# Performance work log

Hardware: AMD Instinct MI355X
Metric: run time of the kernel (lower is better)

## Reference

```python
import jax, jax.numpy as jnp
import numpy as np
import math

B, L, H, NH, DH = 2, 2048, 1024, 16, 64  # batch, seq, hidden, heads, head dim


def setup_inputs() -> dict:
    key = jax.random.key(0)
    ks = jax.random.split(key, 12)
    s = 0.02
    return {
        "v": jax.random.normal(ks[0], (B, L, H), jnp.float32),
        "k": jax.random.normal(ks[1], (B, L, H), jnp.float32),
        "q": jax.random.normal(ks[2], (B, L, H), jnp.float32),
        "mask": jnp.zeros((B, 1, 1, L), jnp.bool_),
        "Wv": jax.random.normal(ks[3], (H, H), jnp.float32) * s,
        "bv": jnp.zeros((H,), jnp.float32),
        "Wk": jax.random.normal(ks[4], (H, H), jnp.float32) * s,
        "bk": jnp.zeros((H,), jnp.float32),
        "Wq": jax.random.normal(ks[5], (H, H), jnp.float32) * s,
        "bq": jnp.zeros((H,), jnp.float32),
        "Wt": jax.random.normal(ks[6], (H, 1), jnp.float32) * s,
        "bt": jnp.zeros((1,), jnp.float32),
        "Wm": jax.random.normal(ks[7], (H, H), jnp.float32) * s,
        "bm": jnp.zeros((H,), jnp.float32),
    }


def reference(v, k, q, mask, Wv, bv, Wk, bk, Wq, bq, Wt, bt, Wm, bm):
    vp = (v @ Wv + bv).reshape(B, L, NH, DH).transpose(0, 2, 1, 3)  # [B,NH,L,DH]
    kp = k @ Wk + bk  # [B,L,H]
    qp = q @ Wq + bq  # [B,L,H]
    threshold = (qp * kp) @ Wt + bt  # [B,L,1] learned per-position gate threshold
    kh = kp.reshape(B, L, NH, DH).transpose(0, 2, 1, 3)  # [B,NH,L,DH]
    qh = qp.reshape(B, L, NH, DH).transpose(0, 2, 1, 3)
    scores = jnp.einsum("bhqd,bhkd->bhqk", qh, kh) / math.sqrt(DH)
    scores = jnp.where(mask, -1e9, scores)
    att_map = jax.nn.softmax(scores, axis=-1)  # [B,NH,Lq,Lk]
    # column sums: over queries (axis -2) then over heads -> [B,Lk,1]
    colsum = att_map.sum(axis=2).sum(axis=1)[..., None]
    a = (colsum - threshold) > 0  # [B,L,1] boolean gate
    atted = jnp.einsum("bhqk,bhkd->bhqd", att_map, vp)  # [B,NH,L,DH]
    atted = atted.transpose(0, 2, 1, 3).reshape(B, L, H)
    atted = atted * a.astype(atted.dtype)
    return atted @ Wm + bm
```

## Files before the change

### kernel.cpp

```cpp
#include <hip/hip_runtime.h>
#include <math.h>

#define BATCH 2
#define SEQ   2048
#define HID   1024
#define NHEAD 16
#define DHEAD 64
#define MROWS (BATCH*SEQ)
#define SCALE_LOG2E 0.1803368801111244f

typedef __attribute__((ext_vector_type(8))) short short8;
typedef __attribute__((ext_vector_type(4))) short short4v;
typedef __attribute__((ext_vector_type(4))) float floatx4;
#define MFMA16(a,b,c) __builtin_amdgcn_mfma_f32_16x16x32_bf16(a,b,c,0,0,0)

extern "C" __device__ float __ocml_native_exp2_f32(float);
#define EXP2F(x) __ocml_native_exp2_f32(x)

#define GLOBAL_TO_LDS16(g, l)                                                  \
    __builtin_amdgcn_global_load_lds(                                          \
        (const __attribute__((address_space(1))) void*)(g),                    \
        (__attribute__((address_space(3))) void*)(l), 16, 0, 0)

__device__ __forceinline__ unsigned short f2bf(float x) {
    union { float f; unsigned u; } v; v.f = x;
    return (unsigned short)((v.u + 0x8000u) >> 16);
}
__device__ __forceinline__ float bf2f(unsigned short s) {
    union { unsigned u; float f; } v; v.u = ((unsigned)s) << 16;
    return v.f;
}
__device__ __forceinline__ unsigned pack_bf16(float lo, float hi) {
    union { float f; unsigned u; } a, b; a.f = lo; b.f = hi;
    return __builtin_amdgcn_perm(b.u + 0x8000u, a.u + 0x8000u, 0x07060302u);
}

__global__ __launch_bounds__(256) void prep_kernel(
    const float* __restrict__ qf, const float* __restrict__ kf,
    const float* __restrict__ vf,
    unsigned short* __restrict__ qa, unsigned short* __restrict__ ka,
    unsigned short* __restrict__ va,
    const float* __restrict__ W0, const float* __restrict__ W1,
    const float* __restrict__ W2, const float* __restrict__ W3,
    unsigned short* __restrict__ T0, unsigned short* __restrict__ T1,
    unsigned short* __restrict__ T2, unsigned short* __restrict__ T3,
    float* __restrict__ colsum)
{
    __shared__ float T[64][68];
    const int bid = blockIdx.x;
    const int tid = threadIdx.x;

    if (bid < 6144) {
        const int which = bid >> 11, pos = bid & 2047;
        const float* in; unsigned short* out;
        switch (which) {
            case 0:  in = qf; out = qa; break;
            case 1:  in = kf; out = ka; break;
            default: in = vf; out = va; break;
        }
        const size_t i = ((size_t)pos * 256 + tid) * 8;
        const float4 a = *(const float4*)&in[i];
        const float4 b = *(const float4*)&in[i + 4];
        uint4 u;
        u.x = pack_bf16(a.x, a.y); u.y = pack_bf16(a.z, a.w);
        u.z = pack_bf16(b.x, b.y); u.w = pack_bf16(b.z, b.w);
        *(uint4*)&out[i] = u;
    } else if (bid < 7168) {
        const int t = bid - 6144;
        const int z = t >> 8;
        const float* W; unsigned short* Wt;
        switch (z) {
            case 0:  W = W0; Wt = T0; break;
            case 1:  W = W1; Wt = T1; break;
            case 2:  W = W2; Wt = T2; break;
            default: W = W3; Wt = T3; break;
        }
        const int k0 = (t & 15) * 64, n0 = ((t >> 4) & 15) * 64;
#pragma unroll
        for (int it = 0; it < 4; it++) {
            const int id = it * 256 + tid;
            const int r = id >> 4, c4 = (id & 15) << 2;
            *(float4*)&T[r][c4] = *(const float4*)&W[(size_t)(k0 + r) * HID + n0 + c4];
        }
        __syncthreads();
#pragma unroll
        for (int it = 0; it < 2; it++) {
            const int id = it * 256 + tid;
            const int n = id >> 3, k8 = (id & 7) << 3;
            uint4 u;
            u.x = pack_bf16(T[k8 + 0][n], T[k8 + 1][n]);
            u.y = pack_bf16(T[k8 + 2][n], T[k8 + 3][n]);
            u.z = pack_bf16(T[k8 + 4][n], T[k8 + 5][n]);
            u.w = pack_bf16(T[k8 + 6][n], T[k8 + 7][n]);
            *(uint4*)&Wt[(size_t)(n0 + n) * HID + k0 + k8] = u;
        }
    } else {
        const int pos = bid - 7168;
        const size_t i = ((size_t)pos * 256 + tid) * 8;
        float4 z4; z4.x = 0.f; z4.y = 0.f; z4.z = 0.f; z4.w = 0.f;
        *(float4*)&colsum[i] = z4;
        *(float4*)&colsum[i + 4] = z4;
    }
}

__global__ __launch_bounds__(256) void proj3_mfma_kernel(
    const unsigned short* __restrict__ A0, const unsigned short* __restrict__ A1,
    const unsigned short* __restrict__ A2,
    const unsigned short* __restrict__ B0, const unsigned short* __restrict__ B1,
    const unsigned short* __restrict__ B2,
    const float* __restrict__ bi0, const float* __restrict__ bi1,
    const float* __restrict__ bi2,
    unsigned short* __restrict__ C0, unsigned short* __restrict__ C1,
    unsigned short* __restrict__ vt)
{
    const unsigned short *Ab, *Bt; const float* bias;
    switch (blockIdx.z) {
        case 0:  Ab = A0; Bt = B0; bias = bi0; break;
        case 1:  Ab = A1; Bt = B1; bias = bi1; break;
        default: Ab = A2; Bt = B2; bias = bi2; break;
    }
    __shared__ unsigned short As[128 * 64];
    __shared__ unsigned short Bs[128 * 64];
    const int tid = threadIdx.x;
    const int w = tid >> 6, lane = tid & 63;
    const int c = lane & 15, quad = lane >> 4;
    const int m0 = blockIdx.x * 128, n0 = blockIdx.y * 128;
    const int wm = (w >> 1) * 64, wn = (w & 1) * 64;
    const int xr = c & 7;

    floatx4 acc[4][4];
#pragma unroll
    for (int i = 0; i < 4; i++)
#pragma unroll
        for (int j = 0; j < 4; j++) acc[i][j] = (floatx4){0.f, 0.f, 0.f, 0.f};

    for (int kc = 0; kc < HID; kc += 64) {
        __syncthreads();
#pragma unroll
        for (int it = 0; it < 4; it++) {
            const int id = it * 256 + tid;
            const int r = id >> 3;
            const int gsw = ((id & 7) ^ (r & 7)) << 3;
            GLOBAL_TO_LDS16(&Ab[(size_t)(m0 + r) * HID + kc + gsw], &As[id << 3]);
            GLOBAL_TO_LDS16(&Bt[(size_t)(n0 + r) * HID + kc + gsw], &Bs[id << 3]);
        }
        __syncthreads();
#pragma unroll
        for (int kk = 0; kk < 2; kk++) {
            short8 af[4], bf[4];
#pragma unroll
            for (int mt = 0; mt < 4; mt++)
                af[mt] = *(const short8*)
                    &As[((wm + mt * 16 + c) << 6) + (((kk * 4 + quad) ^ xr) << 3)];
#pragma unroll
            for (int nt = 0; nt < 4; nt++)
                bf[nt] = *(const short8*)
                    &Bs[((wn + nt * 16 + c) << 6) + (((kk * 4 + quad) ^ xr) << 3)];
#pragma unroll
            for (int mt = 0; mt < 4; mt++)
#pragma unroll
                for (int nt = 0; nt < 4; nt++)
                    acc[mt][nt] = MFMA16(af[mt], bf[nt], acc[mt][nt]);
        }
    }

    if (blockIdx.z < 2) {
        unsigned short* Cb = blockIdx.z == 0 ? C0 : C1;
#pragma unroll
        for (int nt = 0; nt < 4; nt++) {
            const int n = n0 + wn + nt * 16 + c;
            const float bb = bias[n];
#pragma unroll
            for (int mt = 0; mt < 4; mt++) {
                const int m = m0 + wm + mt * 16 + quad * 4;
#pragma unroll
                for (int r = 0; r < 4; r++)
                    Cb[(size_t)(m + r) * HID + n] = f2bf(acc[mt][nt][r] + bb);
            }
        }
    } else {
#pragma unroll
        for (int nt = 0; nt < 4; nt++) {
            const int n = n0 + wn + nt * 16 + c;
            const float bb = bias[n];
            const int h = n >> 6, d = n & 63;
#pragma unroll
            for (int mt = 0; mt < 4; mt++) {
                const int m = m0 + wm + mt * 16 + quad * 4;
                const int b = m >> 11, l = m & 2047;
                ushort4 u;
                u.x = f2bf(acc[mt][nt][0] + bb);
                u.y = f2bf(acc[mt][nt][1] + bb);
                u.z = f2bf(acc[mt][nt][2] + bb);
                u.w = f2bf(acc[mt][nt][3] + bb);
                *(ushort4*)&vt[((size_t)(b * NHEAD + h) * DHEAD + d) * SEQ + l] = u;
            }
        }
    }
}

__global__ __launch_bounds__(256) void gemm_gate_kernel(
    const unsigned short* __restrict__ Ab, const unsigned short* __restrict__ Bt,
    const float* __restrict__ bias,
    const float* __restrict__ gate_cs, const float* __restrict__ gate_th,
    float* __restrict__ Cf)
{
    __shared__ unsigned short As[128 * 64];
    __shared__ unsigned short Bs[128 * 64];
    const int tid = threadIdx.x;
    const int w = tid >> 6, lane = tid & 63;
    const int c = lane & 15, quad = lane >> 4;
    const int m0 = blockIdx.x * 128, n0 = blockIdx.y * 128;
    const int wm = (w >> 1) * 64, wn = (w & 1) * 64;
    const int xr = c & 7;

    floatx4 acc[4][4];
#pragma unroll
    for (int i = 0; i < 4; i++)
#pragma unroll
        for (int j = 0; j < 4; j++) acc[i][j] = (floatx4){0.f, 0.f, 0.f, 0.f};

    for (int kc = 0; kc < HID; kc += 64) {
        __syncthreads();
#pragma unroll
        for (int it = 0; it < 4; it++) {
            const int id = it * 256 + tid;
            const int r = id >> 3;
            const int gsw = ((id & 7) ^ (r & 7)) << 3;
            GLOBAL_TO_LDS16(&Ab[(size_t)(m0 + r) * HID + kc + gsw], &As[id << 3]);
            GLOBAL_TO_LDS16(&Bt[(size_t)(n0 + r) * HID + kc + gsw], &Bs[id << 3]);
        }
        __syncthreads();
#pragma unroll
        for (int kk = 0; kk < 2; kk++) {
            short8 af[4], bf[4];
#pragma unroll
            for (int mt = 0; mt < 4; mt++)
                af[mt] = *(const short8*)
                    &As[((wm + mt * 16 + c) << 6) + (((kk * 4 + quad) ^ xr) << 3)];
#pragma unroll
            for (int nt = 0; nt < 4; nt++)
                bf[nt] = *(const short8*)
                    &Bs[((wn + nt * 16 + c) << 6) + (((kk * 4 + quad) ^ xr) << 3)];
#pragma unroll
            for (int mt = 0; mt < 4; mt++)
#pragma unroll
                for (int nt = 0; nt < 4; nt++)
                    acc[mt][nt] = MFMA16(af[mt], bf[nt], acc[mt][nt]);
        }
    }

    float gmul[4][4];
#pragma unroll
    for (int mt = 0; mt < 4; mt++)
#pragma unroll
        for (int r = 0; r < 4; r++) {
            const int m = m0 + wm + mt * 16 + quad * 4 + r;
            gmul[mt][r] = (gate_cs[m] - gate_th[m]) > 0.f ? 1.f : 0.f;
        }

#pragma unroll
    for (int nt = 0; nt < 4; nt++) {
        const int n = n0 + wn + nt * 16 + c;
        const float bb = bias[n];
#pragma unroll
        for (int mt = 0; mt < 4; mt++) {
            const int m = m0 + wm + mt * 16 + quad * 4;
#pragma unroll
            for (int r = 0; r < 4; r++)
                Cf[(size_t)(m + r) * HID + n] = fmaf(acc[mt][nt][r], gmul[mt][r], bb);
        }
    }
}

__global__ __launch_bounds__(512) void flash_mfma_kernel(
    const unsigned short* __restrict__ qb, const unsigned short* __restrict__ kb,
    const unsigned short* __restrict__ vt, const unsigned char* __restrict__ mask,
    unsigned short* __restrict__ att, float* __restrict__ zinv_out)
{
    const int n = blockIdx.x;
    const int xcd = n & 7, t = n >> 3;
    const int g = xcd + 8 * (t >> 4);
    const int qblk = t & 15;
    const int h = g & 15, b = g >> 4;
    const int q0 = qblk * 128;

    const int tid = threadIdx.x;
    const int w = tid >> 6, lane = tid & 63;
    const int c = lane & 15, quad = lane >> 4;

    __shared__ unsigned short SM[18048];
    unsigned short* Ks = SM;
    unsigned short* Vs = SM + 4608;
    unsigned short* Ps = SM + 9216;
    float* mbf = (float*)(SM + 17920);
    unsigned short* Qs = SM;

    const size_t hoff = (size_t)h * DHEAD;
#pragma unroll
    for (int it = 0; it < 2; it++) {
        const int gg = it * 512 + tid;
        const int r = gg >> 3, c8 = (gg & 7) << 3;
        *(uint4*)&Qs[r * 72 + c8] =
            *(const uint4*)&qb[(size_t)(b * SEQ + q0 + r) * HID + hoff + c8];
    }
    __syncthreads();
    const short8 aq0 = *(const short8*)&Qs[(w * 16 + c) * 72 + quad * 8];
    const short8 aq1 = *(const short8*)&Qs[(w * 16 + c) * 72 + 32 + quad * 8];

    floatx4 acc_o[4];
#pragma unroll
    for (int dt = 0; dt < 4; dt++) acc_o[dt] = (floatx4){0.f, 0.f, 0.f, 0.f};
    float zp[4] = {0.f, 0.f, 0.f, 0.f};
    const size_t vtbase = (size_t)(b * NHEAD + h) * DHEAD * SEQ;

    const int sr = tid >> 3, sc8 = (tid & 7) << 3;
    uint4 kreg = *(const uint4*)&kb[(size_t)(b * SEQ + sr) * HID + hoff + sc8];
    uint4 vreg = *(const uint4*)&vt[vtbase + (size_t)sr * SEQ + sc8];
    float mreg = 0.f;
    if (tid < 64) mreg = mask[(size_t)b * SEQ + tid] ? -1e9f : 0.f;

    for (int kc = 0; kc < SEQ; kc += 64) {
        __syncthreads();
        *(uint4*)&Ks[sr * 72 + sc8] = kreg;
        *(uint4*)&Vs[sr * 72 + sc8] = vreg;
        if (tid < 64) mbf[tid] = mreg;
        __syncthreads();
        if (kc + 64 < SEQ) {
            kreg = *(const uint4*)&kb[(size_t)(b * SEQ + kc + 64 + sr) * HID + hoff + sc8];
            vreg = *(const uint4*)&vt[vtbase + (size_t)sr * SEQ + kc + 64 + sc8];
            if (tid < 64) mreg = mask[(size_t)b * SEQ + kc + 64 + tid] ? -1e9f : 0.f;
        }

#pragma unroll
        for (int nt = 0; nt < 4; nt++) {
            const short8 bk0 = *(const short8*)&Ks[(nt * 16 + c) * 72 + quad * 8];
            const short8 bk1 = *(const short8*)&Ks[(nt * 16 + c) * 72 + 32 + quad * 8];
            floatx4 s = (floatx4){0.f, 0.f, 0.f, 0.f};
            s = MFMA16(aq0, bk0, s);
            s = MFMA16(aq1, bk1, s);
            const float mb = mbf[nt * 16 + c];
#pragma unroll
            for (int r = 0; r < 4; r++) {
                const float p = EXP2F(fmaf(s[r], SCALE_LOG2E, mb));
                zp[r] += p;
                Ps[(w * 16 + quad * 4 + r) * 68 + nt * 16 + c] = f2bf(p);
            }
        }

        const unsigned short* pr = &Ps[(w * 16 + c) * 68];
        short4v p00 = *(const short4v*)&pr[quad * 8];
        short4v p01 = *(const short4v*)&pr[quad * 8 + 4];
        short4v p10 = *(const short4v*)&pr[32 + quad * 8];
        short4v p11 = *(const short4v*)&pr[32 + quad * 8 + 4];
        const short8 ap0 = __builtin_shufflevector(p00, p01, 0, 1, 2, 3, 4, 5, 6, 7);
        const short8 ap1 = __builtin_shufflevector(p10, p11, 0, 1, 2, 3, 4, 5, 6, 7);
#pragma unroll
        for (int dt = 0; dt < 4; dt++) {
            const short8 bv0 = *(const short8*)&Vs[(dt * 16 + c) * 72 + quad * 8];
            const short8 bv1 = *(const short8*)&Vs[(dt * 16 + c) * 72 + 32 + quad * 8];
            acc_o[dt] = MFMA16(ap0, bv0, acc_o[dt]);
            acc_o[dt] = MFMA16(ap1, bv1, acc_o[dt]);
        }
    }

#pragma unroll
    for (int r = 0; r < 4; r++) {
        float z = zp[r];
        z += __shfl_xor(z, 1, 64); z += __shfl_xor(z, 2, 64);
        z += __shfl_xor(z, 4, 64); z += __shfl_xor(z, 8, 64);
        zp[r] = 1.0f / (z + 1e-30f);
    }

#pragma unroll
    for (int dt = 0; dt < 4; dt++)
#pragma unroll
        for (int r = 0; r < 4; r++)
            att[(size_t)(b * SEQ + q0 + w * 16 + quad * 4 + r) * HID + hoff +
                dt * 16 + c] = f2bf(acc_o[dt][r] * zp[r]);

    if (c == 0) {
        const size_t zb = (size_t)(b * NHEAD + h) * SEQ + q0 + w * 16 + quad * 4;
#pragma unroll
        for (int r = 0; r < 4; r++) zinv_out[zb + r] = zp[r];
    }
}

__global__ __launch_bounds__(512) void colsum_thr_kernel(
    const unsigned short* __restrict__ qb, const unsigned short* __restrict__ kb,
    const unsigned char* __restrict__ mask, const float* __restrict__ zinv,
    float* __restrict__ colsum,
    const float* __restrict__ Wt, const float* __restrict__ bt,
    float* __restrict__ thr)
{
    __shared__ unsigned short SM[9216];
    const int tid = threadIdx.x;
    const int w = tid >> 6, lane = tid & 63;

    if (blockIdx.x >= 512) {
        const int row = (blockIdx.x - 512) * 8 + w;
        const unsigned short* qr = qb + (size_t)row * HID;
        const unsigned short* kr = kb + (size_t)row * HID;
        float s = 0.f;
#pragma unroll
        for (int ii = 0; ii < 2; ii++) {
            const int base = ii * 512 + lane * 8;
            const ushort4 q0 = *(const ushort4*)&qr[base];
            const ushort4 q1 = *(const ushort4*)&qr[base + 4];
            const ushort4 k0 = *(const ushort4*)&kr[base];
            const ushort4 k1 = *(const ushort4*)&kr[base + 4];
            const float4 w0 = *(const float4*)&Wt[base];
            const float4 w1 = *(const float4*)&Wt[base + 4];
            s += bf2f(q0.x) * bf2f(k0.x) * w0.x + bf2f(q0.y) * bf2f(k0.y) * w0.y +
                 bf2f(q0.z) * bf2f(k0.z) * w0.z + bf2f(q0.w) * bf2f(k0.w) * w0.w +
                 bf2f(q1.x) * bf2f(k1.x) * w1.x + bf2f(q1.y) * bf2f(k1.y) * w1.y +
                 bf2f(q1.z) * bf2f(k1.z) * w1.z + bf2f(q1.w) * bf2f(k1.w) * w1.w;
        }
#pragma unroll
        for (int off = 32; off > 0; off >>= 1) s += __shfl_xor(s, off, 64);
        if (lane == 0) thr[row] = s + bt[0];
        return;
    }

    const int n = blockIdx.x;
    const int xcd = n & 7, t = n >> 3;
    const int g = xcd + 8 * (t >> 4);
    const int h = g & 15, b = g >> 4;
    const int k0 = (t & 15) * 128;
    const int c = lane & 15, quad = lane >> 4;

    unsigned short* Qs = SM;
    float* zs = (float*)(SM + 4608);
    unsigned short* Kst = SM;

    const size_t hoff = (size_t)h * DHEAD;
#pragma unroll
    for (int it = 0; it < 2; it++) {
        const int gg = it * 512 + tid;
        const int r = gg >> 3, c8 = (gg & 7) << 3;
        *(uint4*)&Kst[r * 72 + c8] =
            *(const uint4*)&kb[(size_t)(b * SEQ + k0 + r) * HID + hoff + c8];
    }
    float mb[4];
#pragma unroll
    for (int r = 0; r < 4; r++)
        mb[r] = mask[(size_t)b * SEQ + k0 + w * 16 + quad * 4 + r] ? -1e9f : 0.f;
    __syncthreads();
    const short8 ak0 = *(const short8*)&Kst[(w * 16 + c) * 72 + quad * 8];
    const short8 ak1 = *(const short8*)&Kst[(w * 16 + c) * 72 + 32 + quad * 8];

    float cs[4] = {0.f, 0.f, 0.f, 0.f};
    const size_t zbase = (size_t)(b * NHEAD + h) * SEQ;

    const int sr = tid >> 3, sc8 = (tid & 7) << 3;
    uint4 qreg = *(const uint4*)&qb[(size_t)(b * SEQ + sr) * HID + hoff + sc8];
    float zreg = 0.f;
    if (tid < 64) zreg = zinv[zbase + tid];

    for (int qc = 0; qc < SEQ; qc += 64) {
        __syncthreads();
        *(uint4*)&Qs[sr * 72 + sc8] = qreg;
        if (tid < 64) zs[tid] = zreg;
        __syncthreads();
        if (qc + 64 < SEQ) {
            qreg = *(const uint4*)&qb[(size_t)(b * SEQ + qc + 64 + sr) * HID + hoff + sc8];
            if (tid < 64) zreg = zinv[zbase + qc + 64 + tid];
        }

#pragma unroll
        for (int qt = 0; qt < 4; qt++) {
            const short8 bq0 = *(const short8*)&Qs[(qt * 16 + c) * 72 + quad * 8];
            const short8 bq1 = *(const short8*)&Qs[(qt * 16 + c) * 72 + 32 + quad * 8];
            floatx4 s = (floatx4){0.f, 0.f, 0.f, 0.f};
            s = MFMA16(ak0, bq0, s);
            s = MFMA16(ak1, bq1, s);
            const float zi = zs[qt * 16 + c];
#pragma unroll
            for (int r = 0; r < 4; r++)
                cs[r] += EXP2F(fmaf(s[r], SCALE_LOG2E, mb[r])) * zi;
        }
    }

#pragma unroll
    for (int r = 0; r < 4; r++) {
        float v = cs[r];
        v += __shfl_xor(v, 1, 64); v += __shfl_xor(v, 2, 64);
        v += __shfl_xor(v, 4, 64); v += __shfl_xor(v, 8, 64);
        if (c == 0)
            atomicAdd(&colsum[(size_t)b * SEQ + k0 + w * 16 + quad * 4 + r], v);
    }
}

extern "C" void kernel_launch(void* const* d_in, const int* in_sizes, int n_in,
                              void* d_out, int out_size, void* d_ws, size_t ws_size,
                              hipStream_t stream)
{
    const float* v  = (const float*)d_in[0];
    const float* k  = (const float*)d_in[1];
    const float* q  = (const float*)d_in[2];
    const unsigned char* mask = (const unsigned char*)d_in[3];
    const float* Wv = (const float*)d_in[4];
    const float* bv = (const float*)d_in[5];
    const float* Wk = (const float*)d_in[6];
    const float* bk = (const float*)d_in[7];
    const float* Wq = (const float*)d_in[8];
    const float* bq = (const float*)d_in[9];
    const float* Wt = (const float*)d_in[10];
    const float* bt = (const float*)d_in[11];
    const float* Wm = (const float*)d_in[12];
    const float* bm = (const float*)d_in[13];
    float* out = (float*)d_out;

    const size_t NE = (size_t)MROWS * HID;
    const size_t WE = (size_t)HID * HID;
    unsigned short* qa   = (unsigned short*)d_ws;
    unsigned short* ka   = qa  + NE;
    unsigned short* va   = ka  + NE;
    unsigned short* qp   = va  + NE;
    unsigned short* kp   = qp  + NE;
    unsigned short* vtb  = kp  + NE;
    unsigned short* WqT  = vtb + NE;
    unsigned short* WkT  = WqT + WE;
    unsigned short* WvT  = WkT + WE;
    unsigned short* WmT  = WvT + WE;
    float* thr    = (float*)(WmT + WE);
    float* zinv   = thr  + MROWS;
    float* colsum = zinv + (size_t)BATCH * NHEAD * SEQ;
    unsigned short* attb = qa;

    prep_kernel<<<7170, 256, 0, stream>>>(q, k, v, qa, ka, va,
                                          Wq, Wk, Wv, Wm, WqT, WkT, WvT, WmT,
                                          colsum);

    proj3_mfma_kernel<<<dim3(MROWS / 128, HID / 128, 3), 256, 0, stream>>>(
        qa, ka, va, WqT, WkT, WvT, bq, bk, bv, qp, kp, vtb);

    flash_mfma_kernel<<<BATCH * NHEAD * (SEQ / 128), 512, 0, stream>>>(
        qp, kp, vtb, mask, attb, zinv);

    colsum_thr_kernel<<<1024, 512, 0, stream>>>(
        qp, kp, mask, zinv, colsum, Wt, bt, thr);

    gemm_gate_kernel<<<dim3(MROWS / 128, HID / 128), 256, 0, stream>>>(
        attb, WmT, bm, colsum, thr, out);
}
```

Baseline: 280.9 us.

## Switch attention and column-sum kernels to 32x32x16 MFMA tiles with split-K waves

```diff
diff --git a/kernel.cpp b/kernel.cpp
--- a/kernel.cpp
+++ b/kernel.cpp
@@ -10,9 +10,10 @@
 #define SCALE_LOG2E 0.1803368801111244f
 
 typedef __attribute__((ext_vector_type(8))) short short8;
-typedef __attribute__((ext_vector_type(4))) short short4v;
 typedef __attribute__((ext_vector_type(4))) float floatx4;
+typedef __attribute__((ext_vector_type(16))) float floatx16;
 #define MFMA16(a,b,c) __builtin_amdgcn_mfma_f32_16x16x32_bf16(a,b,c,0,0,0)
+#define MFMA32(a,b,c) __builtin_amdgcn_mfma_f32_32x32x16_bf16(a,b,c,0,0,0)
 
 extern "C" __device__ float __ocml_native_exp2_f32(float);
 #define EXP2F(x) __ocml_native_exp2_f32(x)
@@ -273,7 +274,7 @@
     }
 }
 
-__global__ __launch_bounds__(512) void flash_mfma_kernel(
+__global__ __launch_bounds__(512, 4) void flash_mfma_kernel(
     const unsigned short* __restrict__ qb, const unsigned short* __restrict__ kb,
     const unsigned short* __restrict__ vt, const unsigned char* __restrict__ mask,
     unsigned short* __restrict__ att, float* __restrict__ zinv_out)
@@ -287,13 +288,15 @@
 
     const int tid = threadIdx.x;
     const int w = tid >> 6, lane = tid & 63;
-    const int c = lane & 15, quad = lane >> 4;
-
-    __shared__ unsigned short SM[18048];
+    const int l31 = lane & 31, lh = lane >> 5;
+    const int qt = w & 3;
+    const int kh = (w >> 2) * 32;
+
+    __shared__ unsigned short SM[19584];
     unsigned short* Ks = SM;
     unsigned short* Vs = SM + 4608;
     unsigned short* Ps = SM + 9216;
-    float* mbf = (float*)(SM + 17920);
+    float* mbf = (float*)(SM + 19456);
     unsigned short* Qs = SM;
 
     const size_t hoff = (size_t)h * DHEAD;
@@ -305,21 +308,25 @@
             *(const uint4*)&qb[(size_t)(b * SEQ + q0 + r) * HID + hoff + c8];
     }
     __syncthreads();
-    const short8 aq0 = *(const short8*)&Qs[(w * 16 + c) * 72 + quad * 8];
-    const short8 aq1 = *(const short8*)&Qs[(w * 16 + c) * 72 + 32 + quad * 8];
-
-    floatx4 acc_o[4];
-#pragma unroll
-    for (int dt = 0; dt < 4; dt++) acc_o[dt] = (floatx4){0.f, 0.f, 0.f, 0.f};
-    float zp[4] = {0.f, 0.f, 0.f, 0.f};
+    short8 aq[4];
+#pragma unroll
+    for (int d0 = 0; d0 < 4; d0++)
+        aq[d0] = *(const short8*)&Qs[(qt * 32 + l31) * 72 + d0 * 16 + lh * 8];
+
+    floatx16 acc0, acc1;
+    float zp[16];
+#pragma unroll
+    for (int r = 0; r < 16; r++) { acc0[r] = 0.f; acc1[r] = 0.f; zp[r] = 0.f; }
+
     const size_t vtbase = (size_t)(b * NHEAD + h) * DHEAD * SEQ;
-
     const int sr = tid >> 3, sc8 = (tid & 7) << 3;
     uint4 kreg = *(const uint4*)&kb[(size_t)(b * SEQ + sr) * HID + hoff + sc8];
     uint4 vreg = *(const uint4*)&vt[vtbase + (size_t)sr * SEQ + sc8];
     float mreg = 0.f;
     if (tid < 64) mreg = mask[(size_t)b * SEQ + tid] ? -1e9f : 0.f;
 
+    unsigned short* Pw = Ps + w * 1280;
+
     for (int kc = 0; kc < SEQ; kc += 64) {
         __syncthreads();
         *(uint4*)&Ks[sr * 72 + sc8] = kreg;
@@ -332,61 +339,73 @@
             if (tid < 64) mreg = mask[(size_t)b * SEQ + kc + 64 + tid] ? -1e9f : 0.f;
         }
 
-#pragma unroll
-        for (int nt = 0; nt < 4; nt++) {
-            const short8 bk0 = *(const short8*)&Ks[(nt * 16 + c) * 72 + quad * 8];
-            const short8 bk1 = *(const short8*)&Ks[(nt * 16 + c) * 72 + 32 + quad * 8];
-            floatx4 s = (floatx4){0.f, 0.f, 0.f, 0.f};
-            s = MFMA16(aq0, bk0, s);
-            s = MFMA16(aq1, bk1, s);
-            const float mb = mbf[nt * 16 + c];
-#pragma unroll
-            for (int r = 0; r < 4; r++) {
-                const float p = EXP2F(fmaf(s[r], SCALE_LOG2E, mb));
-                zp[r] += p;
-                Ps[(w * 16 + quad * 4 + r) * 68 + nt * 16 + c] = f2bf(p);
-            }
-        }
-
-        const unsigned short* pr = &Ps[(w * 16 + c) * 68];
-        short4v p00 = *(const short4v*)&pr[quad * 8];
-        short4v p01 = *(const short4v*)&pr[quad * 8 + 4];
-        short4v p10 = *(const short4v*)&pr[32 + quad * 8];
-        short4v p11 = *(const short4v*)&pr[32 + quad * 8 + 4];
-        const short8 ap0 = __builtin_shufflevector(p00, p01, 0, 1, 2, 3, 4, 5, 6, 7);
-        const short8 ap1 = __builtin_shufflevector(p10, p11, 0, 1, 2, 3, 4, 5, 6, 7);
-#pragma unroll
-        for (int dt = 0; dt < 4; dt++) {
-            const short8 bv0 = *(const short8*)&Vs[(dt * 16 + c) * 72 + quad * 8];
-            const short8 bv1 = *(const short8*)&Vs[(dt * 16 + c) * 72 + 32 + quad * 8];
-            acc_o[dt] = MFMA16(ap0, bv0, acc_o[dt]);
-            acc_o[dt] = MFMA16(ap1, bv1, acc_o[dt]);
-        }
-    }
-
-#pragma unroll
-    for (int r = 0; r < 4; r++) {
+        floatx16 s;
+#pragma unroll
+        for (int r = 0; r < 16; r++) s[r] = 0.f;
+#pragma unroll
+        for (int d0 = 0; d0 < 4; d0++) {
+            const short8 bk = *(const short8*)&Ks[(kh + l31) * 72 + d0 * 16 + lh * 8];
+            s = MFMA32(aq[d0], bk, s);
+        }
+        const float mb = mbf[kh + l31];
+#pragma unroll
+        for (int r = 0; r < 16; r++) {
+            const float p = EXP2F(fmaf(s[r], SCALE_LOG2E, mb));
+            zp[r] += p;
+            const int row = (r & 3) + 8 * (r >> 2) + 4 * lh;
+            Pw[row * 40 + l31] = f2bf(p);
+        }
+
+#pragma unroll
+        for (int k0 = 0; k0 < 2; k0++) {
+            const short8 ap = *(const short8*)&Pw[l31 * 40 + k0 * 16 + lh * 8];
+            const short8 bv0 = *(const short8*)&Vs[l31 * 72 + kh + k0 * 16 + lh * 8];
+            const short8 bv1 = *(const short8*)&Vs[(32 + l31) * 72 + kh + k0 * 16 + lh * 8];
+            acc0 = MFMA32(ap, bv0, acc0);
+            acc1 = MFMA32(ap, bv1, acc1);
+        }
+    }
+
+#pragma unroll
+    for (int r = 0; r < 16; r++) {
         float z = zp[r];
-        z += __shfl_xor(z, 1, 64); z += __shfl_xor(z, 2, 64);
-        z += __shfl_xor(z, 4, 64); z += __shfl_xor(z, 8, 64);
-        zp[r] = 1.0f / (z + 1e-30f);
-    }
-
-#pragma unroll
-    for (int dt = 0; dt < 4; dt++)
-#pragma unroll
-        for (int r = 0; r < 4; r++)
-            att[(size_t)(b * SEQ + q0 + w * 16 + quad * 4 + r) * HID + hoff +
-                dt * 16 + c] = f2bf(acc_o[dt][r] * zp[r]);
-
-    if (c == 0) {
-        const size_t zb = (size_t)(b * NHEAD + h) * SEQ + q0 + w * 16 + quad * 4;
-#pragma unroll
-        for (int r = 0; r < 4; r++) zinv_out[zb + r] = zp[r];
-    }
-}
-
-__global__ __launch_bounds__(512) void colsum_thr_kernel(
+        z += __shfl_xor(z, 1, 64);  z += __shfl_xor(z, 2, 64);
+        z += __shfl_xor(z, 4, 64);  z += __shfl_xor(z, 8, 64);
+        z += __shfl_xor(z, 16, 64);
+        zp[r] = z;
+    }
+
+    __syncthreads();
+    float* Osh = (float*)SM;
+    float* Zsh = (float*)((char*)SM + 32768);
+    if (kh == 0) {
+#pragma unroll
+        for (int r = 0; r < 16; r++) {
+            const int row = (r & 3) + 8 * (r >> 2) + 4 * lh;
+            Osh[(qt * 32 + row) * 64 + l31]      = acc0[r];
+            Osh[(qt * 32 + row) * 64 + 32 + l31] = acc1[r];
+            if (l31 == 0) Zsh[qt * 32 + row] = zp[r];
+        }
+    }
+    __syncthreads();
+    if (kh == 32) {
+#pragma unroll
+        for (int r = 0; r < 16; r++) {
+            const int row = (r & 3) + 8 * (r >> 2) + 4 * lh;
+            const float zt = zp[r] + Zsh[qt * 32 + row];
+            const float zi = 1.0f / (zt + 1e-30f);
+            const float o0 = (acc0[r] + Osh[(qt * 32 + row) * 64 + l31]) * zi;
+            const float o1 = (acc1[r] + Osh[(qt * 32 + row) * 64 + 32 + l31]) * zi;
+            const size_t arow = (size_t)(b * SEQ + q0 + qt * 32 + row) * HID + hoff;
+            att[arow + l31]      = f2bf(o0);
+            att[arow + 32 + l31] = f2bf(o1);
+            if (l31 == 0)
+                zinv_out[(size_t)(b * NHEAD + h) * SEQ + q0 + qt * 32 + row] = zi;
+        }
+    }
+}
+
+__global__ __launch_bounds__(512, 4) void colsum_thr_kernel(
     const unsigned short* __restrict__ qb, const unsigned short* __restrict__ kb,
     const unsigned char* __restrict__ mask, const float* __restrict__ zinv,
     float* __restrict__ colsum,
@@ -427,7 +446,9 @@
     const int g = xcd + 8 * (t >> 4);
     const int h = g & 15, b = g >> 4;
     const int k0 = (t & 15) * 128;
-    const int c = lane & 15, quad = lane >> 4;
+    const int l31 = lane & 31, lh = lane >> 5;
+    const int kt = w & 3;
+    const int qh = (w >> 2) * 32;
 
     unsigned short* Qs = SM;
     float* zs = (float*)(SM + 4608);
@@ -441,15 +462,21 @@
         *(uint4*)&Kst[r * 72 + c8] =
             *(const uint4*)&kb[(size_t)(b * SEQ + k0 + r) * HID + hoff + c8];
     }
-    float mb[4];
-#pragma unroll
-    for (int r = 0; r < 4; r++)
-        mb[r] = mask[(size_t)b * SEQ + k0 + w * 16 + quad * 4 + r] ? -1e9f : 0.f;
     __syncthreads();
-    const short8 ak0 = *(const short8*)&Kst[(w * 16 + c) * 72 + quad * 8];
-    const short8 ak1 = *(const short8*)&Kst[(w * 16 + c) * 72 + 32 + quad * 8];
-
-    float cs[4] = {0.f, 0.f, 0.f, 0.f};
+    short8 ak[4];
+#pragma unroll
+    for (int d0 = 0; d0 < 4; d0++)
+        ak[d0] = *(const short8*)&Kst[(kt * 32 + l31) * 72 + d0 * 16 + lh * 8];
+    float mb[16];
+#pragma unroll
+    for (int r = 0; r < 16; r++) {
+        const int row = (r & 3) + 8 * (r >> 2) + 4 * lh;
+        mb[r] = mask[(size_t)b * SEQ + k0 + kt * 32 + row] ? -1e9f : 0.f;
+    }
+
+    float cs[16];
+#pragma unroll
+    for (int r = 0; r < 16; r++) cs[r] = 0.f;
     const size_t zbase = (size_t)(b * NHEAD + h) * SEQ;
 
     const int sr = tid >> 3, sc8 = (tid & 7) << 3;
@@ -467,27 +494,30 @@
             if (tid < 64) zreg = zinv[zbase + qc + 64 + tid];
         }
 
-#pragma unroll
-        for (int qt = 0; qt < 4; qt++) {
-            const short8 bq0 = *(const short8*)&Qs[(qt * 16 + c) * 72 + quad * 8];
-            const short8 bq1 = *(const short8*)&Qs[(qt * 16 + c) * 72 + 32 + quad * 8];
-            floatx4 s = (floatx4){0.f, 0.f, 0.f, 0.f};
-            s = MFMA16(ak0, bq0, s);
-            s = MFMA16(ak1, bq1, s);
-            const float zi = zs[qt * 16 + c];
-#pragma unroll
-            for (int r = 0; r < 4; r++)
-                cs[r] += EXP2F(fmaf(s[r], SCALE_LOG2E, mb[r])) * zi;
-        }
-    }
-
-#pragma unroll
-    for (int r = 0; r < 4; r++) {
+        floatx16 s;
+#pragma unroll
+        for (int r = 0; r < 16; r++) s[r] = 0.f;
+#pragma unroll
+        for (int d0 = 0; d0 < 4; d0++) {
+            const short8 bq = *(const short8*)&Qs[(qh + l31) * 72 + d0 * 16 + lh * 8];
+            s = MFMA32(ak[d0], bq, s);
+        }
+        const float zi = zs[qh + l31];
+#pragma unroll
+        for (int r = 0; r < 16; r++)
+            cs[r] += EXP2F(fmaf(s[r], SCALE_LOG2E, mb[r])) * zi;
+    }
+
+#pragma unroll
+    for (int r = 0; r < 16; r++) {
         float v = cs[r];
-        v += __shfl_xor(v, 1, 64); v += __shfl_xor(v, 2, 64);
-        v += __shfl_xor(v, 4, 64); v += __shfl_xor(v, 8, 64);
-        if (c == 0)
-            atomicAdd(&colsum[(size_t)b * SEQ + k0 + w * 16 + quad * 4 + r], v);
+        v += __shfl_xor(v, 1, 64);  v += __shfl_xor(v, 2, 64);
+        v += __shfl_xor(v, 4, 64);  v += __shfl_xor(v, 8, 64);
+        v += __shfl_xor(v, 16, 64);
+        if (l31 == 0) {
+            const int row = (r & 3) + 8 * (r >> 2) + 4 * lh;
+            atomicAdd(&colsum[(size_t)b * SEQ + k0 + kt * 32 + row], v);
+        }
     }
 }
 
```

After: 288.3 us. +2.6%, slower.
